# Kernel optimization log

Hardware: AMD Instinct MI355X
Metric: run time of the kernel (lower is better)

Reference implementation:

```python
import jax, jax.numpy as jnp
import numpy as np

BN_EPS = 1e-5


def setup_inputs() -> dict:
    key = jax.random.key(0)
    k0, k1, k2 = jax.random.split(key, 3)
    N, K, Cin, Cout = 300000, 27, 32, 64
    data = jax.random.normal(k0, (N, Cin), dtype=jnp.float32)
    # Octree neighbor table: index of the neighbor node for each of the 27
    # stencil offsets (-1 would mean empty; here all indices are valid).
    neigh = jax.random.randint(k1, (N, K), 0, N, dtype=jnp.int64)
    # Conv weight, one [Cin, Cout] matrix per stencil offset.
    weight = jax.random.normal(k2, (K, Cin, Cout), dtype=jnp.float32) * (1.0 / np.sqrt(K * Cin))
    gamma = jnp.ones((Cout,), dtype=jnp.float32)
    beta = jnp.zeros((Cout,), dtype=jnp.float32)
    return {"data": data, "neigh": neigh, "weight": weight, "gamma": gamma, "beta": beta}


def reference(data, neigh, weight, gamma, beta):
    # --- OctreeConv: gather neighbors (im2col over sparse octree) + matmul ---
    mask = neigh >= 0                                   # [N, K] valid-neighbor mask
    idx = jnp.clip(neigh, 0)
    gathered = jnp.where(mask[..., None], data[idx], 0.0)  # [N, K, Cin]
    out = jnp.einsum('nkc,kco->no', gathered, weight)       # [N, Cout]
    # --- BatchNorm1d (training mode: batch statistics over nodes) ---
    mean = jnp.mean(out, axis=0)
    var = jnp.var(out, axis=0)
    out = (out - mean) * jax.lax.rsqrt(var + BN_EPS) * gamma + beta
    # --- ReLU ---
    return jax.nn.relu(out)
```

## Files before the change

### kernel.cpp

```cpp
#include <hip/hip_runtime.h>

#define N_NODES   300000
#define K_STENCIL 27
#define CIN       32
#define COUT      64
#define BN_EPS    1e-5f

#define WS_STATS_OFF 0
#define WS_AB_OFF    32768
#define WS_WT_OFF    33280
#define N_SPLITS     64

typedef short bf16x8 __attribute__((ext_vector_type(8)));
typedef float f32x4  __attribute__((ext_vector_type(4)));

__device__ __forceinline__ short f2bf_rne(float f) {
    unsigned u = __builtin_bit_cast(unsigned, f);
    u += 0x7fffu + ((u >> 16) & 1u);
    return (short)(u >> 16);
}

__global__ void zero_stats(float* __restrict__ stats) {
    stats[blockIdx.x * blockDim.x + threadIdx.x] = 0.f;
}

__global__ void prep_weight(const float* __restrict__ w, unsigned short* __restrict__ wT) {
    int t = blockIdx.x * blockDim.x + threadIdx.x;
    if (t >= K_STENCIL * COUT * CIN) return;
    int c = t & (CIN - 1);
    int o = (t >> 5) & (COUT - 1);
    int k = t >> 11;
    wT[t] = (unsigned short)f2bf_rne(w[(k * CIN + c) * COUT + o]);
}

__global__ __launch_bounds__(256) void conv_mfma(
        const float* __restrict__ data, const int* __restrict__ neigh,
        const unsigned short* __restrict__ wT, float* __restrict__ out) {
    const int wave  = threadIdx.x >> 6;
    const int lane  = threadIdx.x & 63;
    const int row16 = lane & 15;
    const int quad  = lane >> 4;

    bf16x8 ia, tb;
    #pragma unroll
    for (int j = 0; j < 8; ++j) {
        int k = quad * 8 + j;
        ia[j] = (k == row16) ? (short)0x3F80 : (short)0;
        tb[j] = f2bf_rne((float)(k * 16 + row16));
    }
    f32x4 pacc = {0.f, 0.f, 0.f, 0.f};
    pacc = __builtin_amdgcn_mfma_f32_16x16x32_bf16(ia, tb, pacc, 0, 0, 0);
    int mrow[4], ncol[4];
    #pragma unroll
    for (int r = 0; r < 4; ++r) {
        int iv = (int)(pacc[r] + 0.5f);
        mrow[r] = (iv >> 4) & 15;
        ncol[r] = iv & 15;
    }

    const int node   = blockIdx.x * 64 + wave * 16 + row16;
    const bool valid = (node < N_NODES);
    const int nclamp = valid ? node : 0;

    f32x4 acc[4] = {f32x4{0,0,0,0}, f32x4{0,0,0,0}, f32x4{0,0,0,0}, f32x4{0,0,0,0}};
    const int* nrow = neigh + nclamp * K_STENCIL;

    #pragma unroll 3
    for (int k = 0; k < K_STENCIL; ++k) {
        int idx = nrow[k];
        bf16x8 afrag;
        if (valid && idx >= 0) {
            const f32x4* drow = (const f32x4*)(data + (size_t)idx * CIN + quad * 8);
            f32x4 lo = drow[0];
            f32x4 hi = drow[1];
            #pragma unroll
            for (int j = 0; j < 4; ++j) {
                afrag[j]     = f2bf_rne(lo[j]);
                afrag[j + 4] = f2bf_rne(hi[j]);
            }
        } else {
            afrag = bf16x8{0,0,0,0,0,0,0,0};
        }
        const unsigned short* wk = wT + k * (COUT * CIN) + row16 * CIN + quad * 8;
        #pragma unroll
        for (int ct = 0; ct < 4; ++ct) {
            bf16x8 bfrag = *(const bf16x8*)(wk + ct * 16 * CIN);
            acc[ct] = __builtin_amdgcn_mfma_f32_16x16x32_bf16(afrag, bfrag, acc[ct], 0, 0, 0);
        }
    }

    const int tilebase = blockIdx.x * 64 + wave * 16;
    #pragma unroll
    for (int ct = 0; ct < 4; ++ct) {
        #pragma unroll
        for (int r = 0; r < 4; ++r) {
            int n_out = tilebase + mrow[r];
            if (n_out < N_NODES)
                out[(size_t)n_out * COUT + ct * 16 + ncol[r]] = acc[ct][r];
        }
    }
}

__global__ __launch_bounds__(256) void stats_pass(const float* __restrict__ out,
                                                  float* __restrict__ stats) {
    __shared__ float lsum[COUT];
    __shared__ float lsq[COUT];
    if (threadIdx.x < COUT) { lsum[threadIdx.x] = 0.f; lsq[threadIdx.x] = 0.f; }
    __syncthreads();

    const int j = threadIdx.x & 15;
    int row = blockIdx.x * 16 + (threadIdx.x >> 4);
    const int rstride = gridDim.x * 16;
    float s0=0,s1=0,s2=0,s3=0,q0=0,q1=0,q2=0,q3=0;
    for (; row < N_NODES; row += rstride) {
        f32x4 v = ((const f32x4*)out)[row * 16 + j];
        s0 += v[0]; q0 += v[0]*v[0];
        s1 += v[1]; q1 += v[1]*v[1];
        s2 += v[2]; q2 += v[2]*v[2];
        s3 += v[3]; q3 += v[3]*v[3];
    }
    atomicAdd(&lsum[j*4+0], s0); atomicAdd(&lsq[j*4+0], q0);
    atomicAdd(&lsum[j*4+1], s1); atomicAdd(&lsq[j*4+1], q1);
    atomicAdd(&lsum[j*4+2], s2); atomicAdd(&lsq[j*4+2], q2);
    atomicAdd(&lsum[j*4+3], s3); atomicAdd(&lsq[j*4+3], q3);
    __syncthreads();

    if (threadIdx.x < 128) {
        int split = blockIdx.x & (N_SPLITS - 1);
        float v = (threadIdx.x < 64) ? lsum[threadIdx.x] : lsq[threadIdx.x - 64];
        atomicAdd(&stats[split * 128 + threadIdx.x], v);
    }
}

__global__ void finalize_stats(const float* __restrict__ stats,
                               const float* __restrict__ gamma,
                               const float* __restrict__ beta,
                               float* __restrict__ ab) {
    int o = threadIdx.x;
    if (o >= COUT) return;
    float s = 0.f, q = 0.f;
    for (int sp = 0; sp < N_SPLITS; ++sp) {
        s += stats[sp * 128 + o];
        q += stats[sp * 128 + 64 + o];
    }
    float inv_n = 1.0f / (float)N_NODES;
    float mean = s * inv_n;
    float var  = q * inv_n - mean * mean;
    float a = gamma[o] * rsqrtf(var + BN_EPS);
    float b = beta[o] - mean * a;
    ab[o] = a;
    ab[64 + o] = b;
}

__global__ __launch_bounds__(256) void bn_relu(float* __restrict__ out,
                                               const float* __restrict__ ab) {
    int i = blockIdx.x * blockDim.x + threadIdx.x;
    f32x4 a = ((const f32x4*)ab)[i & 15];
    f32x4 b = ((const f32x4*)(ab + 64))[i & 15];
    f32x4 v = ((f32x4*)out)[i];
    #pragma unroll
    for (int j = 0; j < 4; ++j) {
        float y = v[j] * a[j] + b[j];
        v[j] = y > 0.f ? y : 0.f;
    }
    ((f32x4*)out)[i] = v;
}

extern "C" void kernel_launch(void* const* d_in, const int* in_sizes, int n_in,
                              void* d_out, int out_size, void* d_ws, size_t ws_size,
                              hipStream_t stream) {
    const float* data   = (const float*)d_in[0];
    const int*   neigh  = (const int*)d_in[1];
    const float* weight = (const float*)d_in[2];
    const float* gamma  = (const float*)d_in[3];
    const float* beta   = (const float*)d_in[4];
    float* out = (float*)d_out;

    char* ws = (char*)d_ws;
    float*          stats = (float*)(ws + WS_STATS_OFF);
    float*          ab    = (float*)(ws + WS_AB_OFF);
    unsigned short* wT    = (unsigned short*)(ws + WS_WT_OFF);

    zero_stats<<<32, 256, 0, stream>>>(stats);
    prep_weight<<<(K_STENCIL * COUT * CIN + 255) / 256, 256, 0, stream>>>(weight, wT);

    int grid = (N_NODES + 63) / 64;
    conv_mfma<<<grid, 256, 0, stream>>>(data, neigh, wT, out);

    stats_pass<<<1024, 256, 0, stream>>>(out, stats);
    finalize_stats<<<1, 64, 0, stream>>>(stats, gamma, beta, ab);

    int total4 = N_NODES * COUT / 4;
    bn_relu<<<total4 / 256, 256, 0, stream>>>(out, ab);
}
```

Baseline: 412.4 us.

## Pre-convert data to bf16 and fuse BN statistics into conv epilogue

```diff
diff --git a/kernel.cpp b/kernel.cpp
--- a/kernel.cpp
+++ b/kernel.cpp
@@ -9,9 +9,12 @@
 #define WS_STATS_OFF 0
 #define WS_AB_OFF    32768
 #define WS_WT_OFF    33280
+#define WS_DATAB_OFF 147456
+#define WS_NEEDED    (WS_DATAB_OFF + (size_t)N_NODES * CIN * 2)
 #define N_SPLITS     64
 
 typedef short bf16x8 __attribute__((ext_vector_type(8)));
+typedef short bf16x4 __attribute__((ext_vector_type(4)));
 typedef float f32x4  __attribute__((ext_vector_type(4)));
 
 __device__ __forceinline__ short f2bf_rne(float f) {
@@ -33,7 +36,92 @@
     wT[t] = (unsigned short)f2bf_rne(w[(k * CIN + c) * COUT + o]);
 }
 
-__global__ __launch_bounds__(256) void conv_mfma(
+__global__ __launch_bounds__(256) void prep_data(const float* __restrict__ d,
+                                                 unsigned short* __restrict__ o) {
+    int i = blockIdx.x * blockDim.x + threadIdx.x;
+    f32x4 v = ((const f32x4*)d)[i];
+    bf16x4 r;
+    #pragma unroll
+    for (int j = 0; j < 4; ++j) r[j] = f2bf_rne(v[j]);
+    ((bf16x4*)o)[i] = r;
+}
+
+__global__ __launch_bounds__(256) void conv_mfma_b(
+        const unsigned short* __restrict__ dataB, const int* __restrict__ neigh,
+        const unsigned short* __restrict__ wT, float* __restrict__ out,
+        float* __restrict__ stats) {
+    __shared__ float lsum[COUT];
+    __shared__ float lsq[COUT];
+    if (threadIdx.x < COUT) { lsum[threadIdx.x] = 0.f; lsq[threadIdx.x] = 0.f; }
+    __syncthreads();
+
+    const int wave  = threadIdx.x >> 6;
+    const int lane  = threadIdx.x & 63;
+    const int row16 = lane & 15;
+    const int quad  = lane >> 4;
+
+    bf16x8 ia, tb;
+    #pragma unroll
+    for (int j = 0; j < 8; ++j) {
+        int k = quad * 8 + j;
+        ia[j] = (k == row16) ? (short)0x3F80 : (short)0;
+        tb[j] = f2bf_rne((float)(k * 16 + row16));
+    }
+    f32x4 pacc = {0.f, 0.f, 0.f, 0.f};
+    pacc = __builtin_amdgcn_mfma_f32_16x16x32_bf16(ia, tb, pacc, 0, 0, 0);
+    int mrow[4], ncol[4];
+    #pragma unroll
+    for (int r = 0; r < 4; ++r) {
+        int iv = (int)(pacc[r] + 0.5f);
+        mrow[r] = (iv >> 4) & 15;
+        ncol[r] = iv & 15;
+    }
+
+    const int node   = blockIdx.x * 64 + wave * 16 + row16;
+    const bool valid = (node < N_NODES);
+    const int nclamp = valid ? node : 0;
+
+    f32x4 acc[4] = {f32x4{0,0,0,0}, f32x4{0,0,0,0}, f32x4{0,0,0,0}, f32x4{0,0,0,0}};
+    const int* nrow = neigh + nclamp * K_STENCIL;
+
+    #pragma unroll 9
+    for (int k = 0; k < K_STENCIL; ++k) {
+        int idx = nrow[k];
+        bf16x8 afrag = bf16x8{0,0,0,0,0,0,0,0};
+        if (valid && idx >= 0)
+            afrag = *(const bf16x8*)(dataB + (size_t)idx * CIN + quad * 8);
+        const unsigned short* wk = wT + k * (COUT * CIN) + row16 * CIN + quad * 8;
+        #pragma unroll
+        for (int ct = 0; ct < 4; ++ct) {
+            bf16x8 bfrag = *(const bf16x8*)(wk + ct * 16 * CIN);
+            acc[ct] = __builtin_amdgcn_mfma_f32_16x16x32_bf16(afrag, bfrag, acc[ct], 0, 0, 0);
+        }
+    }
+
+    const int tilebase = blockIdx.x * 64 + wave * 16;
+    #pragma unroll
+    for (int ct = 0; ct < 4; ++ct) {
+        #pragma unroll
+        for (int r = 0; r < 4; ++r) {
+            int n_out = tilebase + mrow[r];
+            float v = acc[ct][r];
+            if (n_out < N_NODES) {
+                out[(size_t)n_out * COUT + ct * 16 + ncol[r]] = v;
+                atomicAdd(&lsum[ct * 16 + ncol[r]], v);
+                atomicAdd(&lsq [ct * 16 + ncol[r]], v * v);
+            }
+        }
+    }
+
+    __syncthreads();
+    if (threadIdx.x < 128) {
+        int split = blockIdx.x & (N_SPLITS - 1);
+        float v = (threadIdx.x < 64) ? lsum[threadIdx.x] : lsq[threadIdx.x - 64];
+        atomicAdd(&stats[split * 128 + threadIdx.x], v);
+    }
+}
+
+__global__ __launch_bounds__(256) void conv_mfma_f(
         const float* __restrict__ data, const int* __restrict__ neigh,
         const unsigned short* __restrict__ wT, float* __restrict__ out) {
     const int wave  = threadIdx.x >> 6;
@@ -180,14 +268,20 @@
     float*          stats = (float*)(ws + WS_STATS_OFF);
     float*          ab    = (float*)(ws + WS_AB_OFF);
     unsigned short* wT    = (unsigned short*)(ws + WS_WT_OFF);
+    unsigned short* dataB = (unsigned short*)(ws + WS_DATAB_OFF);
 
     zero_stats<<<32, 256, 0, stream>>>(stats);
     prep_weight<<<(K_STENCIL * COUT * CIN + 255) / 256, 256, 0, stream>>>(weight, wT);
 
-    int grid = (N_NODES + 63) / 64;
-    conv_mfma<<<grid, 256, 0, stream>>>(data, neigh, wT, out);
-
-    stats_pass<<<1024, 256, 0, stream>>>(out, stats);
+    const int grid = (N_NODES + 63) / 64;
+    if (ws_size >= WS_NEEDED) {
+        prep_data<<<N_NODES * CIN / 4 / 256, 256, 0, stream>>>(data, dataB);
+        conv_mfma_b<<<grid, 256, 0, stream>>>(dataB, neigh, wT, out, stats);
+    } else {
+        conv_mfma_f<<<grid, 256, 0, stream>>>(data, neigh, wT, out);
+        stats_pass<<<1024, 256, 0, stream>>>(out, stats);
+    }
+
     finalize_stats<<<1, 64, 0, stream>>>(stats, gamma, beta, ab);
 
     int total4 = N_NODES * COUT / 4;
```

Result: slower. 468.2 us (+13.5%).
